# Kernel optimization log

Measured on AMD Instinct MI355X. Metric: run time of the kernel, lower is better.

## Reference

```python
import jax, jax.numpy as jnp
import numpy as np

B, H, W = 16, 96, 96
KS = (5, 3, 3)          # kernel sizes per layer
PD = (2, 1, 1)          # paddings per layer
PCT = (0.5, 0.5, 0.4)   # triangle_cReLU percent per layer
C1, C2, C3 = 64, 128, 256
ALPHA = jnp.linspace(0.9, 0.99, 4, dtype=jnp.float32).reshape(2, 2)  # SFM alpha (not trained)


def extract_patches(x, k, s, p):
    # x: (B,C,H,W) -> (B, Ho*Wo, C*k*k), torch.unfold ordering (C slowest)
    x = jnp.pad(x, ((0, 0), (0, 0), (p, p), (p, p)))
    b, c, h, w = x.shape
    ho, wo = (h - k) // s + 1, (w - k) // s + 1
    I = (jnp.arange(ho) * s)[:, None, None, None] + jnp.arange(k)[None, None, :, None]
    J = (jnp.arange(wo) * s)[None, :, None, None] + jnp.arange(k)[None, None, None, :]
    pt = x[:, :, I, J]                      # (B,C,Ho,Wo,k,k)
    pt = pt.transpose(0, 2, 3, 1, 4, 5).reshape(b, ho * wo, c * k * k)
    return pt, ho, wo


def rbf_conv(x, Wt, k, s, p):
    # torch: cdist(unfold(x), W) -> (B, O, Ho, Wo)
    pt, ho, wo = extract_patches(x, k, s, p)
    d2 = (jnp.sum(pt * pt, -1)[:, :, None]
          + jnp.sum(Wt * Wt, -1)[None, None, :]
          - 2.0 * jnp.einsum('bpk,ok->bpo', pt, Wt))
    d = jnp.sqrt(jnp.maximum(d2, 1e-12))
    return d.transpose(0, 2, 1).reshape(x.shape[0], Wt.shape[0], ho, wo)


def triangle_crelu(d, w, percent):
    # threshold = int((1-percent)*C)-th largest over channel dim, capped at w
    c = d.shape[1]
    k = int((1.0 - percent) * c)
    dt = jnp.transpose(d, (0, 2, 3, 1))           # (B,H,W,C)
    thr = jax.lax.top_k(dt, k)[0][..., k - 1]     # (B,H,W)
    thr = jnp.minimum(thr, w)[:, None, :, :]
    d = jnp.where(d > thr, w, d)
    return 1.0 - d / w


def sfm(x, f):
    # non-overlapping fxf weighted-mean pooling with alpha weights
    b, c, h, w = x.shape
    xb = x.reshape(b, c, h // f, f, w // f, f).transpose(0, 1, 2, 4, 3, 5)
    return jnp.mean(xb * ALPHA, axis=(-2, -1))


def branch(xc, W1, W2, W3, wv):
    # xc: (B,H,W) single color channel; wv: (3,) triangle w per layer
    x = xc[:, None]                                   # (B,1,H,W)
    x = rbf_conv(x, W1, KS[0], 1, PD[0])
    x = triangle_crelu(x, wv[0], PCT[0])
    x = sfm(x, 2)                                     # (B,64,48,48)
    x = rbf_conv(x, W2, KS[1], 1, PD[1])
    x = triangle_crelu(x, wv[1], PCT[1])
    x = sfm(x, 2)                                     # (B,128,24,24)
    x = rbf_conv(x, W3, KS[2], 1, PD[2])
    x = triangle_crelu(x, wv[2], PCT[2])              # (B,256,24,24)
    return x


def setup_inputs() -> dict:
    key = jax.random.key(0)
    ks = jax.random.split(key, 8)

    def kaiming(k, shape):
        bound = float(np.sqrt(6.0 / shape[-1]))
        return jax.random.uniform(k, shape, jnp.float32, -bound, bound)

    x = jax.random.normal(ks[0], (B, 3, H, W), jnp.float32)
    conv_w1 = kaiming(ks[1], (3, C1, 1 * KS[0] * KS[0]))    # per-branch RBF prototypes
    conv_w2 = kaiming(ks[2], (3, C2, C1 * KS[1] * KS[1]))
    conv_w3 = kaiming(ks[3], (3, C3, C2 * KS[2] * KS[2]))
    tri_w = jnp.tile(jnp.array([0.4, 0.4, 4.0], jnp.float32), (3, 1))  # (branch, layer)
    fc_in = 3 * C3 * 24 * 24
    fc_w = jax.random.normal(ks[4], (10, fc_in), jnp.float32) * 0.01
    fc_b = jnp.zeros((10,), jnp.float32)
    return {"x": x, "conv_w1": conv_w1, "conv_w2": conv_w2, "conv_w3": conv_w3,
            "tri_w": tri_w, "fc_w": fc_w, "fc_b": fc_b}


def reference(x, conv_w1, conv_w2, conv_w3, tri_w, fc_w, fc_b):
    xs = jnp.transpose(x, (1, 0, 2, 3))                       # (3,B,H,W)
    feats = jax.vmap(branch)(xs, conv_w1, conv_w2, conv_w3, tri_w)  # (3,B,256,24,24)
    flat = jnp.transpose(feats, (1, 0, 2, 3, 4)).reshape(x.shape[0], -1)
    return flat @ fc_w.T + fc_b
```

## Files before the change

### kernel.cpp

```cpp
#include <hip/hip_runtime.h>
#include <hip/hip_bf16.h>
#include <math.h>

typedef __attribute__((ext_vector_type(8))) short bf16x8;
typedef __attribute__((ext_vector_type(4))) float f32x4;

__device__ __forceinline__ void bsplit(float f, unsigned short& h,
                                       unsigned short& l) {
  __hip_bfloat16 hb = __float2bfloat16(f);
  float hf = __bfloat162float(hb);
  __hip_bfloat16 lb = __float2bfloat16(f - hf);
  h = *reinterpret_cast<unsigned short*>(&hb);
  l = *reinterpret_cast<unsigned short*>(&lb);
}

template <int CIN, int COUT>
__global__ __launch_bounds__(256) void pack_w_kernel(
    const float* __restrict__ w, unsigned short* __restrict__ bph,
    unsigned short* __restrict__ bpl, float* __restrict__ sout) {
  constexpr int K = CIN * 9;
  constexpr int CC = CIN / 32;
  const int n = blockIdx.x, br = blockIdx.z;
  const int t = threadIdx.x;
  __shared__ float row[K];
  __shared__ float red[256];
  const float* src = w + ((size_t)br * COUT + n) * K;
  float ss = 0.f;
  for (int i = t; i < K; i += 256) {
    float f = src[i];
    row[i] = f;
    ss += f * f;
  }
  red[t] = ss;
  __syncthreads();
  for (int st = 128; st > 0; st >>= 1) {
    if (t < st) red[t] += red[t + st];
    __syncthreads();
  }
  if (t == 0) sout[br * COUT + n] = red[0];
  for (int i = t; i < K; i += 256) {
    int kpos = i / CIN;
    int e = i - kpos * CIN;
    float f = row[e * 9 + kpos];
    unsigned short h, l;
    bsplit(f, h, l);
    size_t oidx =
        (((size_t)br * 9 * CC + (size_t)kpos * CC + (e >> 5)) * COUT + n) * 32 +
        (e & 31);
    bph[oidx] = h;
    bpl[oidx] = l;
  }
}

__global__ __launch_bounds__(256) void pack_w1_prep_kernel(
    const float* __restrict__ w1, const float* __restrict__ s2,
    const float* __restrict__ s3, const float* __restrict__ tri,
    unsigned short* __restrict__ bh, unsigned short* __restrict__ bl,
    float* __restrict__ s1, float* __restrict__ po0_2,
    float* __restrict__ sp0_2, float* __restrict__ act0_3) {
  const int blk = blockIdx.x;
  const int t = threadIdx.x;
  if (blk < 24) {
    int idx = blk * 256 + t;
    int k = idx & 31;
    int col = (idx >> 5) & 63;
    int br = idx >> 11;
    float f = (k < 31 && k < 25) ? w1[(br * 64 + col) * 25 + k] : 0.f;
    unsigned short h, l;
    bsplit(f, h, l);
    bh[idx] = h;
    bl[idx] = l;
    float v = f * f;
#pragma unroll
    for (int off = 16; off > 0; off >>= 1) v += __shfl_xor(v, off, 64);
    if ((t & 31) == 0) s1[br * 64 + col] = v;
    return;
  }
  if (t >= 64) return;
  const int lane = t;
  if (blk < 27) {
    const int br = blk - 24;
    const float w_ = tri[br * 3 + 1];
    float d0 = sqrtf(fmaxf(s2[br * 128 + lane * 2], 1e-12f));
    float d1 = sqrtf(fmaxf(s2[br * 128 + lane * 2 + 1], 1e-12f));
    int cnt = __popcll(__ballot(d0 >= w_)) + __popcll(__ballot(d1 >= w_));
    float thr;
    if (cnt > 63) {
      thr = w_;
    } else {
      unsigned int k0 = __float_as_uint(d0), k1 = __float_as_uint(d1);
      unsigned int pre = 0;
      int rem = 63;
      for (int b = 30; b >= 0; --b) {
        unsigned int top = (pre >> b) | 1u;
        int c = __popcll(__ballot((k0 >> b) == top)) +
                __popcll(__ballot((k1 >> b) == top));
        if (c > rem) pre |= (1u << b);
        else rem -= c;
      }
      thr = __uint_as_float(pre);
    }
    float th = fminf(thr, w_);
    float a0 = 1.f - ((d0 > th) ? w_ : d0) / w_;
    float a1v = 1.f - ((d1 > th) ? w_ : d1) / w_;
    float p0 = a0 * 0.945f, p1 = a1v * 0.945f;
    po0_2[br * 128 + lane * 2] = p0;
    po0_2[br * 128 + lane * 2 + 1] = p1;
    float ss = p0 * p0 + p1 * p1;
#pragma unroll
    for (int off = 32; off > 0; off >>= 1) ss += __shfl_down(ss, off, 64);
    if (lane == 0) sp0_2[br] = ss;
  } else {
    const int br = blk - 27;
    const float w_ = tri[br * 3 + 2];
    float d[4];
#pragma unroll
    for (int j = 0; j < 4; j++)
      d[j] = sqrtf(fmaxf(s3[br * 256 + lane * 4 + j], 1e-12f));
    int cnt = 0;
#pragma unroll
    for (int j = 0; j < 4; j++) cnt += __popcll(__ballot(d[j] >= w_));
    float thr;
    if (cnt > 152) {
      thr = w_;
    } else {
      unsigned int k[4];
#pragma unroll
      for (int j = 0; j < 4; j++) k[j] = __float_as_uint(d[j]);
      unsigned int pre = 0;
      int rem = 152;
      for (int b = 30; b >= 0; --b) {
        unsigned int top = (pre >> b) | 1u;
        int c = 0;
#pragma unroll
        for (int j = 0; j < 4; j++)
          c += __popcll(__ballot((k[j] >> b) == top));
        if (c > rem) pre |= (1u << b);
        else rem -= c;
      }
      thr = __uint_as_float(pre);
    }
    float th = fminf(thr, w_);
#pragma unroll
    for (int j = 0; j < 4; j++)
      act0_3[br * 256 + lane * 4 + j] = 1.f - ((d[j] > th) ? w_ : d[j]) / w_;
  }
}

__global__ __launch_bounds__(256) void layer1_kernel(
    const float* __restrict__ x, const unsigned short* __restrict__ bw1h,
    const unsigned short* __restrict__ bw1l, const float* __restrict__ sw2v,
    const float* __restrict__ tri, float* __restrict__ a1,
    char* __restrict__ zf1) {
  const int gidx = blockIdx.x;
  const int gy = gidx / 12, gx = gidx % 12;
  const int n = blockIdx.y, br = blockIdx.z;
  const int t = threadIdx.x;
  const int lane = t & 63, wid = t >> 6;

  __shared__ __align__(16) float win[12][12];
  __shared__ float sp2s[64];
  __shared__ float sw2s[64];
  __shared__ __align__(16) float dmat[64][68];

  const int y0 = gy * 8 - 2, x0 = gx * 8 - 2;
  const float* xb = x + ((size_t)(n * 3 + br)) * 96 * 96;
  if (t < 144) {
    int wy = t / 12, wx = t - (t / 12) * 12;
    int y = y0 + wy, xx = x0 + wx;
    float v = 0.f;
    if (y >= 0 && y < 96 && xx >= 0 && xx < 96) v = xb[y * 96 + xx];
    win[wy][wx] = v;
  }
  if (t >= 192) sw2s[t - 192] = sw2v[br * 64 + (t - 192)];
  __syncthreads();

  if (t < 64) {
    int py = t >> 3, px = t & 7;
    float s = 0.f;
#pragma unroll
    for (int ky = 0; ky < 5; ky++)
#pragma unroll
      for (int kx = 0; kx < 5; kx++) {
        float v = win[py + ky][px + kx];
        s += v * v;
      }
    sp2s[t] = s;
  }

  const int mrow = lane & 15;
  const int slot = lane >> 4;
  const int pixel = wid * 16 + mrow;
  const int ppy = pixel >> 3, ppx = pixel & 7;
  unsigned short ahv[8], alv[8];
#pragma unroll
  for (int j = 0; j < 8; j++) {
    int k = slot * 8 + j;
    float v = 0.f;
    if (k < 25) {
      int ky = (k * 205) >> 10;
      int kx = k - ky * 5;
      v = win[ppy + ky][ppx + kx];
    }
    bsplit(v, ahv[j], alv[j]);
  }
  bf16x8 ah = *reinterpret_cast<bf16x8*>(ahv);
  bf16x8 al = *reinterpret_cast<bf16x8*>(alv);

  f32x4 acc[4], accB[4];
  f32x4 zz = {0.f, 0.f, 0.f, 0.f};
#pragma unroll
  for (int nt = 0; nt < 4; nt++) {
    acc[nt] = zz;
    accB[nt] = zz;
  }
#pragma unroll
  for (int nt = 0; nt < 4; nt++) {
    const int off = ((br * 64 + nt * 16 + mrow) << 5) + (slot << 3);
    bf16x8 bh = *reinterpret_cast<const bf16x8*>(bw1h + off);
    bf16x8 bl = *reinterpret_cast<const bf16x8*>(bw1l + off);
    acc[nt] = __builtin_amdgcn_mfma_f32_16x16x32_bf16(ah, bh, acc[nt], 0, 0, 0);
    accB[nt] =
        __builtin_amdgcn_mfma_f32_16x16x32_bf16(ah, bl, accB[nt], 0, 0, 0);
    accB[nt] =
        __builtin_amdgcn_mfma_f32_16x16x32_bf16(al, bh, accB[nt], 0, 0, 0);
  }
  __syncthreads();

  const float w_ = tri[br * 3 + 0];
  const float w2_ = w_ * w_;
  const int flidx = ((br * 16 + n) * 48 + gy * 4 + wid) * 12 + gx;

  float d2v[4][4];
#pragma unroll
  for (int nt = 0; nt < 4; nt++) {
    const float swc = sw2s[nt * 16 + mrow];
#pragma unroll
    for (int rg = 0; rg < 4; rg++)
      d2v[nt][rg] = sp2s[wid * 16 + slot * 4 + rg] + swc -
                    2.f * (acc[nt][rg] + accB[nt][rg]);
  }

  int cnt_lt[4] = {0, 0, 0, 0};
#pragma unroll
  for (int rg = 0; rg < 4; rg++) {
#pragma unroll
    for (int nt = 0; nt < 4; nt++) {
      unsigned long long m = __ballot(d2v[nt][rg] < w2_);
      cnt_lt[rg] += __popcll((m >> (slot * 16)) & 0xFFFFull);
    }
  }

  const bool myzero = (cnt_lt[0] | cnt_lt[1] | cnt_lt[2] | cnt_lt[3]) == 0;
  if (__all(myzero)) {
    if (lane == 0) zf1[flidx] = 0;
    return;
  }

  const float A2[2][2] = {{0.9f, 0.93f}, {0.96f, 0.99f}};
  const bool mycheap = cnt_lt[0] <= 32 && cnt_lt[1] <= 32 &&
                       cnt_lt[2] <= 32 && cnt_lt[3] <= 32;
  if (__all(mycheap)) {
#pragma unroll
    for (int nt = 0; nt < 4; nt++) {
      const int ch = nt * 16 + mrow;
#pragma unroll
      for (int rg = 0; rg < 4; rg++) {
        const int p = wid * 16 + slot * 4 + rg;
        float d2 = d2v[nt][rg];
        float a = (d2 < w2_) ? 1.f - sqrtf(fmaxf(d2, 1e-12f)) / w_ : 0.f;
        dmat[p][ch] = a;
      }
    }
    float pooled[4];
#pragma unroll
    for (int g = 0; g < 4; g++) {
      float po = 0.f;
#pragma unroll
      for (int py = 0; py < 2; py++)
#pragma unroll
        for (int q = 0; q < 2; q++) {
          int pi = py * 8 + g * 2 + q;
          po += dmat[wid * 16 + pi][lane] * A2[py][q];
        }
      pooled[g] = po * 0.25f;
    }
    bool nz = (pooled[0] != 0.f) | (pooled[1] != 0.f) | (pooled[2] != 0.f) |
              (pooled[3] != 0.f);
    unsigned long long mm = __ballot(nz);
    if (mm) {
#pragma unroll
      for (int g = 0; g < 4; g++)
        a1[((((size_t)(br * 16 + n)) * 48 + (gy * 4 + wid)) * 48 +
            (gx * 4 + g)) * 64 + lane] = pooled[g];
      if (lane == 0) zf1[flidx] = 1;
    } else {
      if (lane == 0) zf1[flidx] = 0;
    }
    return;
  }

#pragma unroll
  for (int nt = 0; nt < 4; nt++) {
    const int ch = nt * 16 + mrow;
#pragma unroll
    for (int rg = 0; rg < 4; rg++) {
      const int p = wid * 16 + slot * 4 + rg;
      dmat[p][ch] = sqrtf(fmaxf(d2v[nt][rg], 1e-12f));
    }
  }
  float thrv[16];
  unsigned int need = 0;
#pragma unroll
  for (int i = 0; i < 16; i++) {
    float v = dmat[wid * 16 + i][lane];
    int cnt = __popcll(__ballot(v >= w_));
    if (cnt >= 32) thrv[i] = w_;
    else need |= (1u << i);
  }
  if (need) {
#pragma unroll
    for (int i = 0; i < 16; i++) {
      if (!((need >> i) & 1)) continue;
      unsigned int key = __float_as_uint(dmat[wid * 16 + i][lane]);
      unsigned int pre = 0;
      int rem = 31;
      for (int b = 30; b >= 0; --b) {
        unsigned int top = (pre >> b) | 1u;
        int cnt = __popcll(__ballot((key >> b) == top));
        if (cnt > rem) pre |= (1u << b);
        else rem -= cnt;
      }
      thrv[i] = __uint_as_float(pre);
    }
  }
  float pooled[4];
#pragma unroll
  for (int g = 0; g < 4; g++) {
    float po = 0.f;
#pragma unroll
    for (int py = 0; py < 2; py++)
#pragma unroll
      for (int q = 0; q < 2; q++) {
        int pi = py * 8 + g * 2 + q;
        float d = dmat[wid * 16 + pi][lane];
        float th = fminf(thrv[pi], w_);
        float a = 1.f - ((d > th) ? w_ : d) / w_;
        po += a * A2[py][q];
      }
    pooled[g] = po * 0.25f;
  }
  bool nz = (pooled[0] != 0.f) | (pooled[1] != 0.f) | (pooled[2] != 0.f) |
            (pooled[3] != 0.f);
  unsigned long long mm = __ballot(nz);
  if (mm) {
#pragma unroll
    for (int g = 0; g < 4; g++)
      a1[((((size_t)(br * 16 + n)) * 48 + (gy * 4 + wid)) * 48 +
          (gx * 4 + g)) * 64 + lane] = pooled[g];
    if (lane == 0) zf1[flidx] = 1;
  } else {
    if (lane == 0) zf1[flidx] = 0;
  }
}

__global__ __launch_bounds__(256) void rbf_l2(
    const float* __restrict__ a1, const unsigned short* __restrict__ bph,
    const unsigned short* __restrict__ bpl, const float* __restrict__ sw2v,
    const float* __restrict__ tri, const char* __restrict__ zf1,
    const float* __restrict__ po0_2, char* __restrict__ zf2,
    float* __restrict__ a2) {
  constexpr int CIN = 64, COUT = 128, HIN = 48, KRANK = 63;
  constexpr int CC = CIN / 32, NCH = 9 * CC, NTW = 2, PADC = COUT + 4;
  constexpr int WIN_USH = 60 * CIN;
  constexpr int WIN_BYTES = 2 * WIN_USH * 2;
  constexpr int DMAT_BYTES = 32 * PADC * 4;
  constexpr int UNI_BYTES = WIN_BYTES > DMAT_BYTES ? WIN_BYTES : DMAT_BYTES;

  __shared__ __align__(16) char uni[UNI_BYTES];
  __shared__ float cellq[60][4];
  __shared__ float cellsum[60];
  __shared__ float sp2[32];
  __shared__ float thrs[32];
  __shared__ float sw2s[COUT];
  __shared__ float po0s[COUT];
  __shared__ char fl[24];
  __shared__ int anyf, zflag, diffl;

  unsigned short* winh = (unsigned short*)uni;
  unsigned short* winl = winh + WIN_USH;
  float* dmat = (float*)uni;

  const int gy = blockIdx.x / 6, gx = blockIdx.x % 6;
  const int n = blockIdx.y, br = blockIdx.z;
  const int t = threadIdx.x, lane = t & 63, wvid = t >> 6, ng = wvid;
  const float w_ = tri[br * 3 + 1];
  const int y0 = gy * 4 - 1, x0 = gx * 8 - 1;
  const int fbase = ((br * 16 + n) * 12 + gy) * 6 + gx;

  if (t < 24) {
    int i = t >> 2, j = t & 3;
    int r = gy * 4 - 1 + i, ct = 2 * gx - 1 + j;
    fl[t] = (r >= 0 && r < 48 && ct >= 0 && ct < 12)
                ? zf1[((br * 16 + n) * 48 + r) * 12 + ct]
                : (char)0;
  }
  if (t == 255) diffl = 0;
  __syncthreads();
  if (t == 0) {
    int a = 0;
    for (int i = 0; i < 24; i++) a |= fl[i];
    anyf = a;
  }
  __syncthreads();
  if (!anyf) {
    if (t == 0) zf2[fbase] = 0;
    return;
  }

  for (int i = t; i < COUT; i += 256) {
    sw2s[i] = sw2v[br * COUT + i];
    po0s[i] = po0_2[br * COUT + i];
  }

  const int cell = t >> 2, q = t & 3;
  const int wy = cell / 10, wx = cell - (cell / 10) * 10;
  const int yy = y0 + wy, xx = x0 + wx;
  bool ok = false;
  if (t < 240 && yy >= 0 && yy < HIN && xx >= 0 && xx < HIN)
    ok = fl[wy * 4 + ((xx >> 2) - (2 * gx - 1))] != 0;
  if (t < 240) {
    const float* rp =
        a1 + ((size_t)((br * 16 + n) * HIN + yy) * HIN + xx) * CIN +
        q * (CIN / 4);
    const int sx = (wx & 7) << 3;
    float ss = 0.f;
#pragma unroll
    for (int cq = 0; cq < CIN / 16; cq++) {
      float4 v = ok ? *reinterpret_cast<const float4*>(rp + cq * 4)
                    : make_float4(0.f, 0.f, 0.f, 0.f);
      unsigned short hh[4], ll[4];
      float fv[4] = {v.x, v.y, v.z, v.w};
#pragma unroll
      for (int j = 0; j < 4; j++) {
        float f = fv[j];
        ss += f * f;
        bsplit(f, hh[j], ll[j]);
      }
      int c = q * (CIN / 4) + cq * 4;
      int cst = c ^ sx;
      *reinterpret_cast<ushort4*>(&winh[cell * CIN + cst]) =
          make_ushort4(hh[0], hh[1], hh[2], hh[3]);
      *reinterpret_cast<ushort4*>(&winl[cell * CIN + cst]) =
          make_ushort4(ll[0], ll[1], ll[2], ll[3]);
    }
    cellq[cell][q] = ss;
  }
  __syncthreads();
  if (t < 60)
    cellsum[t] = cellq[t][0] + cellq[t][1] + cellq[t][2] + cellq[t][3];
  __syncthreads();
  if (t < 32) {
    int py = t >> 3, px = t & 7;
    float s = 0.f;
#pragma unroll
    for (int ky = 0; ky < 3; ky++)
#pragma unroll
      for (int kx = 0; kx < 3; kx++) s += cellsum[(py + ky) * 10 + px + kx];
    sp2[t] = s;
  }
  if (t == 0) {
    float s = 0.f;
    for (int i = 0; i < 60; i++) s += cellsum[i];
    zflag = (s == 0.f);
  }
  __syncthreads();
  if (zflag) {
    if (t == 0) zf2[fbase] = 0;
    return;
  }

  const int pix0 = lane & 15;
  const int g8 = (lane >> 4) << 3;
  const int ppy = pix0 >> 3, ppx = pix0 & 7;

  f32x4 acc[2][NTW], accB[2][NTW];
  f32x4 zz = {0.f, 0.f, 0.f, 0.f};
#pragma unroll
  for (int mt = 0; mt < 2; mt++)
#pragma unroll
    for (int nt = 0; nt < NTW; nt++) {
      acc[mt][nt] = zz;
      accB[mt][nt] = zz;
    }

  const size_t bbase = (size_t)br * NCH;
  const int nb0 = ng * (NTW * 16) + pix0;
  bf16x8 bufA[2 * NTW], bufB[2 * NTW], bufC[2 * NTW];

  auto loadB = [&](int chunk, bf16x8* dst) {
    const unsigned short* p0 = bph + ((bbase + chunk) * COUT + nb0) * 32 + g8;
    const unsigned short* p1 = bpl + ((bbase + chunk) * COUT + nb0) * 32 + g8;
#pragma unroll
    for (int nt = 0; nt < NTW; nt++) {
      dst[2 * nt] = *reinterpret_cast<const bf16x8*>(p0 + nt * 512);
      dst[2 * nt + 1] = *reinterpret_cast<const bf16x8*>(p1 + nt * 512);
    }
  };
  auto compute = [&](int chunk, bf16x8* b) {
    const int kpos = chunk / CC, cc = chunk - (chunk / CC) * CC;
    const int ky = kpos / 3, kx = kpos - (kpos / 3) * 3;
    const int wxx = ppx + kx;
    const int sx = (wxx & 7) << 3;
    const int cbase = ((cc << 5) + g8) ^ sx;
#pragma unroll
    for (int mt = 0; mt < 2; mt++) {
      const int r0 = (mt * 2 + ppy + ky) * 10 + wxx;
      bf16x8 ah = *reinterpret_cast<const bf16x8*>(&winh[r0 * CIN + cbase]);
      bf16x8 al = *reinterpret_cast<const bf16x8*>(&winl[r0 * CIN + cbase]);
#pragma unroll
      for (int nt = 0; nt < NTW; nt++) {
        acc[mt][nt] = __builtin_amdgcn_mfma_f32_16x16x32_bf16(
            ah, b[2 * nt], acc[mt][nt], 0, 0, 0);
        accB[mt][nt] = __builtin_amdgcn_mfma_f32_16x16x32_bf16(
            ah, b[2 * nt + 1], accB[mt][nt], 0, 0, 0);
        accB[mt][nt] = __builtin_amdgcn_mfma_f32_16x16x32_bf16(
            al, b[2 * nt], accB[mt][nt], 0, 0, 0);
      }
    }
  };

  loadB(0, bufA);
  loadB(1, bufB);
  for (int g = 0; g < NCH; g += 3) {
    if (g + 2 < NCH) loadB(g + 2, bufC);
    compute(g, bufA);
    if (g + 3 < NCH) loadB(g + 3, bufA);
    compute(g + 1, bufB);
    if (g + 4 < NCH) loadB(g + 4, bufB);
    compute(g + 2, bufC);
  }
  __syncthreads();

  const int rgrp = (lane >> 4) << 2;
#pragma unroll
  for (int mt = 0; mt < 2; mt++) {
    const int prow = mt * 16 + rgrp;
#pragma unroll
    for (int nt = 0; nt < NTW; nt++) {
      const int col = ng * (NTW * 16) + nt * 16 + pix0;
      const float sw = sw2s[col];
#pragma unroll
      for (int rg = 0; rg < 4; rg++) {
        const int pix = prow + rg;
        float d2 =
            sp2[pix] + sw - 2.f * (acc[mt][nt][rg] + accB[mt][nt][rg]);
        dmat[pix * PADC + col] = sqrtf(fmaxf(d2, 1e-12f));
      }
    }
  }
  __syncthreads();

  for (int i = 0; i < 8; i++) {
    const int p = wvid * 8 + i;
    float2 f = *reinterpret_cast<const float2*>(&dmat[p * PADC + lane * 2]);
    float v0 = f.x, v1 = f.y;
    int cnt = __popcll(__ballot(v0 >= w_)) + __popcll(__ballot(v1 >= w_));
    if (cnt > KRANK) {
      if (lane == 0) thrs[p] = w_;
      continue;
    }
    unsigned int k0 = __float_as_uint(v0), k1 = __float_as_uint(v1);
    unsigned int pre = 0;
    int rem = KRANK;
    for (int b = 30; b >= 0; --b) {
      unsigned int top = (pre >> b) | 1u;
      int c = __popcll(__ballot((k0 >> b) == top)) +
              __popcll(__ballot((k1 >> b) == top));
      if (c > rem) pre |= (1u << b);
      else rem -= c;
    }
    if (lane == 0) thrs[p] = __uint_as_float(pre);
  }
  __syncthreads();

  float* ob = a2 + ((size_t)(br * 16 + n)) * 24 * 24 * COUT;
  int mydiff = 0;
  for (int i = t; i < 8 * COUT; i += 256) {
    int qq = i / COUT;
    int chn = i - qq * COUT;
    int qy = qq >> 2, qx = qq & 3;
    int p00 = qy * 16 + qx * 2;
    float d00 = dmat[p00 * PADC + chn];
    float d01 = dmat[(p00 + 1) * PADC + chn];
    float d10 = dmat[(p00 + 8) * PADC + chn];
    float d11 = dmat[(p00 + 9) * PADC + chn];
    float t00 = fminf(thrs[p00], w_);
    float t01 = fminf(thrs[p00 + 1], w_);
    float t10 = fminf(thrs[p00 + 8], w_);
    float t11 = fminf(thrs[p00 + 9], w_);
    float a00 = 1.f - ((d00 > t00) ? w_ : d00) / w_;
    float a01 = 1.f - ((d01 > t01) ? w_ : d01) / w_;
    float a10 = 1.f - ((d10 > t10) ? w_ : d10) / w_;
    float a11 = 1.f - ((d11 > t11) ? w_ : d11) / w_;
    float po = 0.25f * (a00 * 0.9f + a01 * 0.93f + a10 * 0.96f + a11 * 0.99f);
    ob[((size_t)((gy * 2 + qy) * 24 + gx * 4 + qx)) * COUT + chn] = po;
    mydiff |= (po != po0s[chn]);
  }
  if (mydiff) diffl = 1;
  __syncthreads();
  if (t == 0) zf2[fbase] = diffl ? 1 : 0;
}

__global__ __launch_bounds__(256) void rbf_l3(
    const float* __restrict__ a2, const unsigned short* __restrict__ bph,
    const unsigned short* __restrict__ bpl, const float* __restrict__ sw2v,
    const float* __restrict__ tri, const char* __restrict__ zf2,
    const float* __restrict__ po0_2, const float* __restrict__ sp0_2,
    const float* __restrict__ act0_3, unsigned short* __restrict__ fT) {
  constexpr int CIN = 128, COUT = 256, HIN = 24, KRANK = 152;
  constexpr int CC = CIN / 32, NCH = 9 * CC, NTW = 4, PADC = COUT + 4;
  constexpr int WIN_USH = 60 * CIN;
  constexpr int WIN_BYTES = 2 * WIN_USH * 2;
  constexpr int DMAT_BYTES = 32 * PADC * 4;
  constexpr int UNI_BYTES = WIN_BYTES > DMAT_BYTES ? WIN_BYTES : DMAT_BYTES;

  __shared__ __align__(16) char uni[UNI_BYTES];
  __shared__ float cellq[60][4];
  __shared__ float cellsum[60];
  __shared__ float sp2[32];
  __shared__ float thrs[32];
  __shared__ float sw2s[COUT];
  __shared__ __align__(16) float po0s[128];
  __shared__ char fl[16];
  __shared__ int pure0, zflag;

  unsigned short* winh = (unsigned short*)uni;
  unsigned short* winl = winh + WIN_USH;
  float* dmat = (float*)uni;

  const int gy = blockIdx.x / 3, gx = blockIdx.x % 3;
  const int n = blockIdx.y, br = blockIdx.z;
  const int t = threadIdx.x, lane = t & 63, wvid = t >> 6, ng = wvid;
  const float w_ = tri[br * 3 + 2];
  const int y0 = gy * 4 - 1, x0 = gx * 8 - 1;
  const float sp0 = sp0_2[br];

  if (t < 16) {
    int i = t >> 2, j = t & 3;
    int tr = 2 * gy - 1 + i, tc = 2 * gx - 1 + j;
    fl[t] = (tr >= 0 && tr < 12 && tc >= 0 && tc < 6)
                ? zf2[((br * 16 + n) * 12 + tr) * 6 + tc]
                : (char)0;
  }
  if (t >= 64 && t < 192) po0s[t - 64] = po0_2[br * 128 + (t - 64)];
  __syncthreads();
  if (t == 0) {
    int a = 0;
    for (int i = 0; i < 16; i++) a |= fl[i];
    pure0 = (!a) && (sp0 == 0.f);
  }
  __syncthreads();

  unsigned short* obT = fT + (size_t)(br * 16 + n) * 256 * 576;
  if (pure0) {
    int col = t;
    float a = act0_3[br * 256 + col];
    unsigned short h, l;
    bsplit(a, h, l);
    unsigned int hh = (unsigned int)h | ((unsigned int)h << 16);
    uint4 hv = {hh, hh, hh, hh};
#pragma unroll
    for (int row = 0; row < 4; row++)
      *reinterpret_cast<uint4*>(obT + (size_t)col * 576 +
                                (gy * 4 + row) * 24 + gx * 8) = hv;
    return;
  }

  for (int i = t; i < COUT; i += 256) sw2s[i] = sw2v[br * COUT + i];

  const int cell = t >> 2, q = t & 3;
  const int wy = cell / 10, wx = cell - (cell / 10) * 10;
  const int yy = y0 + wy, xx = x0 + wx;
  const bool okb =
      (t < 240) && (yy >= 0 && yy < HIN && xx >= 0 && xx < HIN);
  int fcell = 0;
  if (okb)
    fcell = fl[((yy >> 1) - (2 * gy - 1)) * 4 + ((xx >> 2) - (2 * gx - 1))];
  if (t < 240) {
    const float* rp =
        a2 + ((size_t)((br * 16 + n) * HIN + yy) * HIN + xx) * CIN +
        q * (CIN / 4);
    const int sx = (wx & 7) << 3;
    float ss = 0.f;
#pragma unroll
    for (int cq = 0; cq < CIN / 16; cq++) {
      int c = q * (CIN / 4) + cq * 4;
      float4 v;
      if (!okb) v = make_float4(0.f, 0.f, 0.f, 0.f);
      else if (!fcell) v = *reinterpret_cast<const float4*>(&po0s[c]);
      else v = *reinterpret_cast<const float4*>(rp + cq * 4);
      unsigned short hh[4], ll[4];
      float fv[4] = {v.x, v.y, v.z, v.w};
#pragma unroll
      for (int j = 0; j < 4; j++) {
        float f = fv[j];
        ss += f * f;
        bsplit(f, hh[j], ll[j]);
      }
      int cst = c ^ sx;
      *reinterpret_cast<ushort4*>(&winh[cell * CIN + cst]) =
          make_ushort4(hh[0], hh[1], hh[2], hh[3]);
      *reinterpret_cast<ushort4*>(&winl[cell * CIN + cst]) =
          make_ushort4(ll[0], ll[1], ll[2], ll[3]);
    }
    cellq[cell][q] = ss;
  }
  __syncthreads();
  if (t < 60)
    cellsum[t] = cellq[t][0] + cellq[t][1] + cellq[t][2] + cellq[t][3];
  __syncthreads();
  if (t < 32) {
    int py = t >> 3, px = t & 7;
    float s = 0.f;
#pragma unroll
    for (int ky = 0; ky < 3; ky++)
#pragma unroll
      for (int kx = 0; kx < 3; kx++) s += cellsum[(py + ky) * 10 + px + kx];
    sp2[t] = s;
  }
  if (t == 0) {
    float s = 0.f;
    for (int i = 0; i < 60; i++) s += cellsum[i];
    zflag = (s == 0.f);
  }
  __syncthreads();
  if (zflag) {
    int col = t;
    float a = act0_3[br * 256 + col];
    unsigned short h, l;
    bsplit(a, h, l);
    unsigned int hh = (unsigned int)h | ((unsigned int)h << 16);
    uint4 hv = {hh, hh, hh, hh};
#pragma unroll
    for (int row = 0; row < 4; row++)
      *reinterpret_cast<uint4*>(obT + (size_t)col * 576 +
                                (gy * 4 + row) * 24 + gx * 8) = hv;
    return;
  }

  const int pix0 = lane & 15;
  const int g8 = (lane >> 4) << 3;
  const int ppy = pix0 >> 3, ppx = pix0 & 7;

  f32x4 acc[2][NTW], accB[2][NTW];
  f32x4 zz = {0.f, 0.f, 0.f, 0.f};
#pragma unroll
  for (int mt = 0; mt < 2; mt++)
#pragma unroll
    for (int nt = 0; nt < NTW; nt++) {
      acc[mt][nt] = zz;
      accB[mt][nt] = zz;
    }

  const size_t bbase = (size_t)br * NCH;
  const int nb0 = ng * (NTW * 16) + pix0;
  bf16x8 bufA[2 * NTW], bufB[2 * NTW], bufC[2 * NTW];

  auto loadB = [&](int chunk, bf16x8* dst) {
    const unsigned short* p0 = bph + ((bbase + chunk) * COUT + nb0) * 32 + g8;
    const unsigned short* p1 = bpl + ((bbase + chunk) * COUT + nb0) * 32 + g8;
#pragma unroll
    for (int nt = 0; nt < NTW; nt++) {
      dst[2 * nt] = *reinterpret_cast<const bf16x8*>(p0 + nt * 512);
      dst[2 * nt + 1] = *reinterpret_cast<const bf16x8*>(p1 + nt * 512);
    }
  };
  auto compute = [&](int chunk, bf16x8* b) {
    const int kpos = chunk / CC, cc = chunk - (chunk / CC) * CC;
    const int ky = kpos / 3, kx = kpos - (kpos / 3) * 3;
    const int wxx = ppx + kx;
    const int sx = (wxx & 7) << 3;
    const int cbase = ((cc << 5) + g8) ^ sx;
#pragma unroll
    for (int mt = 0; mt < 2; mt++) {
      const int r0 = (mt * 2 + ppy + ky) * 10 + wxx;
      bf16x8 ah = *reinterpret_cast<const bf16x8*>(&winh[r0 * CIN + cbase]);
      bf16x8 al = *reinterpret_cast<const bf16x8*>(&winl[r0 * CIN + cbase]);
#pragma unroll
      for (int nt = 0; nt < NTW; nt++) {
        acc[mt][nt] = __builtin_amdgcn_mfma_f32_16x16x32_bf16(
            ah, b[2 * nt], acc[mt][nt], 0, 0, 0);
        accB[mt][nt] = __builtin_amdgcn_mfma_f32_16x16x32_bf16(
            ah, b[2 * nt + 1], accB[mt][nt], 0, 0, 0);
        accB[mt][nt] = __builtin_amdgcn_mfma_f32_16x16x32_bf16(
            al, b[2 * nt], accB[mt][nt], 0, 0, 0);
      }
    }
  };

  loadB(0, bufA);
  loadB(1, bufB);
  for (int g = 0; g < NCH; g += 3) {
    if (g + 2 < NCH) loadB(g + 2, bufC);
    compute(g, bufA);
    if (g + 3 < NCH) loadB(g + 3, bufA);
    compute(g + 1, bufB);
    if (g + 4 < NCH) loadB(g + 4, bufB);
    compute(g + 2, bufC);
  }
  __syncthreads();

  const int rgrp = (lane >> 4) << 2;
#pragma unroll
  for (int mt = 0; mt < 2; mt++) {
    const int prow = mt * 16 + rgrp;
#pragma unroll
    for (int nt = 0; nt < NTW; nt++) {
      const int col = ng * (NTW * 16) + nt * 16 + pix0;
      const float sw = sw2s[col];
#pragma unroll
      for (int rg = 0; rg < 4; rg++) {
        const int pix = prow + rg;
        float d2 =
            sp2[pix] + sw - 2.f * (acc[mt][nt][rg] + accB[mt][nt][rg]);
        dmat[pix * PADC + col] = sqrtf(fmaxf(d2, 1e-12f));
      }
    }
  }
  __syncthreads();

  for (int i = 0; i < 8; i++) {
    const int p = wvid * 8 + i;
    float4 f = *reinterpret_cast<const float4*>(&dmat[p * PADC + lane * 4]);
    float v0 = f.x, v1 = f.y, v2 = f.z, v3 = f.w;
    int cnt = __popcll(__ballot(v0 >= w_)) + __popcll(__ballot(v1 >= w_)) +
              __popcll(__ballot(v2 >= w_)) + __popcll(__ballot(v3 >= w_));
    if (cnt > KRANK) {
      if (lane == 0) thrs[p] = w_;
      continue;
    }
    unsigned int k0 = __float_as_uint(v0), k1 = __float_as_uint(v1);
    unsigned int k2 = __float_as_uint(v2), k3 = __float_as_uint(v3);
    unsigned int pre = 0;
    int rem = KRANK;
    for (int b = 30; b >= 0; --b) {
      unsigned int top = (pre >> b) | 1u;
      int c = __popcll(__ballot((k0 >> b) == top)) +
              __popcll(__ballot((k1 >> b) == top)) +
              __popcll(__ballot((k2 >> b) == top)) +
              __popcll(__ballot((k3 >> b) == top));
      if (c > rem) pre |= (1u << b);
      else rem -= c;
    }
    if (lane == 0) thrs[p] = __uint_as_float(pre);
  }
  __syncthreads();

  for (int item = t; item < 256 * 4; item += 256) {
    int chn = item & 255;
    int rowq = item >> 8;
    __align__(16) unsigned short hv[8];
#pragma unroll
    for (int px = 0; px < 8; px++) {
      int p = rowq * 8 + px;
      float d = dmat[p * PADC + chn];
      float tt = fminf(thrs[p], w_);
      float a = 1.f - ((d > tt) ? w_ : d) / w_;
      unsigned short h, l;
      bsplit(a, h, l);
      hv[px] = h;
    }
    *reinterpret_cast<uint4*>(obT + (size_t)chn * 576 +
                              (gy * 4 + rowq) * 24 + gx * 8) =
        *reinterpret_cast<uint4*>(hv);
  }
}

__global__ __launch_bounds__(64) void fc_mfma_kernel(
    const unsigned short* __restrict__ fT, const float* __restrict__ fcw,
    float* __restrict__ partial) {
  const int blk = blockIdx.x;
  const int lane = threadIdx.x;
  const int mrow = lane & 15;
  const int slot = lane >> 4;
  const int slot8 = slot * 8;
  const int k0base = blk * 256;

  f32x4 acc = {0.f, 0.f, 0.f, 0.f};
  float4 z4 = make_float4(0.f, 0.f, 0.f, 0.f);
  for (int cc = 0; cc < 8; ++cc) {
    int k0 = k0base + cc * 32;
    int br = k0 / 147456;
    int rb = k0 - br * 147456;
    int c = rb / 576;
    int pth = rb - c * 576;
    size_t aoff = ((size_t)(br * 16 + mrow) * 256 + c) * 576 + pth + slot8;
    bf16x8 ah = *reinterpret_cast<const bf16x8*>(fT + aoff);
    float4 b0 = z4, b1q = z4;
    if (mrow < 10) {
      const float* bp = fcw + (size_t)mrow * 442368 + k0 + slot8;
      b0 = *reinterpret_cast<const float4*>(bp);
      b1q = *reinterpret_cast<const float4*>(bp + 4);
    }
    float bf[8] = {b0.x, b0.y, b0.z, b0.w, b1q.x, b1q.y, b1q.z, b1q.w};
    unsigned short bhv[8], blv[8];
#pragma unroll
    for (int j = 0; j < 8; j++) bsplit(bf[j], bhv[j], blv[j]);
    bf16x8 bh = *reinterpret_cast<bf16x8*>(bhv);
    bf16x8 bl = *reinterpret_cast<bf16x8*>(blv);
    acc = __builtin_amdgcn_mfma_f32_16x16x32_bf16(ah, bh, acc, 0, 0, 0);
    acc = __builtin_amdgcn_mfma_f32_16x16x32_bf16(ah, bl, acc, 0, 0, 0);
  }
#pragma unroll
  for (int rg = 0; rg < 4; rg++)
    partial[(size_t)blk * 256 + (slot * 4 + rg) * 16 + mrow] = acc[rg];
}

__global__ __launch_bounds__(64) void fc_final_kernel(
    const float* __restrict__ partial, const float* __restrict__ fcb,
    float* __restrict__ outp) {
  const int n = blockIdx.x / 10, oo = blockIdx.x % 10;
  const int lane = threadIdx.x;
  float s = 0.f;
  for (int b = lane; b < 1728; b += 64)
    s += partial[(size_t)b * 256 + n * 16 + oo];
#pragma unroll
  for (int off = 32; off > 0; off >>= 1) s += __shfl_down(s, off, 64);
  if (lane == 0) outp[n * 10 + oo] = s + fcb[oo];
}

extern "C" void kernel_launch(void* const* d_in, const int* in_sizes, int n_in,
                              void* d_out, int out_size, void* d_ws,
                              size_t ws_size, hipStream_t stream) {
  const float* x   = (const float*)d_in[0];
  const float* w1  = (const float*)d_in[1];
  const float* w2  = (const float*)d_in[2];
  const float* w3  = (const float*)d_in[3];
  const float* tri = (const float*)d_in[4];
  const float* fcw = (const float*)d_in[5];
  const float* fcb = (const float*)d_in[6];
  float* out = (float*)d_out;

  float* ws = (float*)d_ws;
  float* a1      = ws;
  float* a2      = a1 + 7077888;
  float* s1      = a2 + 3538944;
  float* s2      = s1 + 192;
  float* s3      = s2 + 384;
  float* po0_2   = s3 + 768;
  float* sp0_2   = po0_2 + 384;
  float* act0_3  = sp0_2 + 16;
  float* partial = act0_3 + 768;
  unsigned short* fT   = (unsigned short*)(partial + 442368);
  unsigned short* bw1h = fT + 7077888;
  unsigned short* bw1l = bw1h + 6144;
  unsigned short* bph2 = bw1l + 6144;
  unsigned short* bpl2 = bph2 + 221184;
  unsigned short* bph3 = bpl2 + 221184;
  unsigned short* bpl3 = bph3 + 884736;
  char* zf1 = (char*)(bpl3 + 884736);
  char* zf2 = zf1 + 27648;

  pack_w_kernel<64, 128><<<dim3(128, 1, 3), dim3(256), 0, stream>>>(
      w2, bph2, bpl2, s2);
  pack_w_kernel<128, 256><<<dim3(256, 1, 3), dim3(256), 0, stream>>>(
      w3, bph3, bpl3, s3);
  pack_w1_prep_kernel<<<dim3(30), dim3(256), 0, stream>>>(
      w1, s2, s3, tri, bw1h, bw1l, s1, po0_2, sp0_2, act0_3);

  layer1_kernel<<<dim3(144, 16, 3), dim3(256), 0, stream>>>(x, bw1h, bw1l, s1,
                                                            tri, a1, zf1);
  rbf_l2<<<dim3(72, 16, 3), dim3(256), 0, stream>>>(a1, bph2, bpl2, s2, tri,
                                                    zf1, po0_2, zf2, a2);
  rbf_l3<<<dim3(18, 16, 3), dim3(256), 0, stream>>>(a2, bph3, bpl3, s3, tri,
                                                    zf2, po0_2, sp0_2, act0_3,
                                                    fT);
  fc_mfma_kernel<<<dim3(1728), dim3(64), 0, stream>>>(fT, fcw, partial);
  fc_final_kernel<<<dim3(160), dim3(64), 0, stream>>>(partial, fcb, out);
}
```

Measured before the change: 71.51 us.

## Double rbf_l2 tile height to 8 input rows per block

Each rbf_l2 block now covers 8 input rows (64 pixels) instead of 4, and the grid is halved. The halo load (10x10 window) and the packed-weight B loads are amortized over twice the MFMA work, cutting redundant window rows and weight fetches. The cost is larger shared memory (window and dmat), twice the accumulator registers, and fewer blocks in flight, which may reduce occupancy. The zero flags are now written for two tiles per block.

```diff
diff --git a/kernel.cpp b/kernel.cpp
--- a/kernel.cpp
+++ b/kernel.cpp
@@ -65,7 +65,7 @@
     int k = idx & 31;
     int col = (idx >> 5) & 63;
     int br = idx >> 11;
-    float f = (k < 31 && k < 25) ? w1[(br * 64 + col) * 25 + k] : 0.f;
+    float f = (k < 25) ? w1[(br * 64 + col) * 25 + k] : 0.f;
     unsigned short h, l;
     bsplit(f, h, l);
     bh[idx] = h;
@@ -372,20 +372,21 @@
     float* __restrict__ a2) {
   constexpr int CIN = 64, COUT = 128, HIN = 48, KRANK = 63;
   constexpr int CC = CIN / 32, NCH = 9 * CC, NTW = 2, PADC = COUT + 4;
-  constexpr int WIN_USH = 60 * CIN;
+  constexpr int WIN_USH = 100 * CIN;
   constexpr int WIN_BYTES = 2 * WIN_USH * 2;
-  constexpr int DMAT_BYTES = 32 * PADC * 4;
+  constexpr int DMAT_BYTES = 64 * PADC * 4;
   constexpr int UNI_BYTES = WIN_BYTES > DMAT_BYTES ? WIN_BYTES : DMAT_BYTES;
 
   __shared__ __align__(16) char uni[UNI_BYTES];
-  __shared__ float cellq[60][4];
-  __shared__ float cellsum[60];
-  __shared__ float sp2[32];
-  __shared__ float thrs[32];
+  __shared__ float cellq[100][2];
+  __shared__ float cellsum[100];
+  __shared__ float sp2[64];
+  __shared__ float thrs[64];
   __shared__ float sw2s[COUT];
   __shared__ float po0s[COUT];
-  __shared__ char fl[24];
-  __shared__ int anyf, zflag, diffl;
+  __shared__ char fl[40];
+  __shared__ int anyf, zflag;
+  __shared__ int diff2[2];
 
   unsigned short* winh = (unsigned short*)uni;
   unsigned short* winl = winh + WIN_USH;
@@ -395,26 +396,30 @@
   const int n = blockIdx.y, br = blockIdx.z;
   const int t = threadIdx.x, lane = t & 63, wvid = t >> 6, ng = wvid;
   const float w_ = tri[br * 3 + 1];
-  const int y0 = gy * 4 - 1, x0 = gx * 8 - 1;
-  const int fbase = ((br * 16 + n) * 12 + gy) * 6 + gx;
-
-  if (t < 24) {
+  const int y0 = gy * 8 - 1, x0 = gx * 8 - 1;
+  const int fbase0 = ((br * 16 + n) * 12 + 2 * gy) * 6 + gx;
+
+  if (t < 40) {
     int i = t >> 2, j = t & 3;
-    int r = gy * 4 - 1 + i, ct = 2 * gx - 1 + j;
+    int r = y0 + i, ct = 2 * gx - 1 + j;
     fl[t] = (r >= 0 && r < 48 && ct >= 0 && ct < 12)
                 ? zf1[((br * 16 + n) * 48 + r) * 12 + ct]
                 : (char)0;
   }
-  if (t == 255) diffl = 0;
+  if (t == 254) diff2[0] = 0;
+  if (t == 255) diff2[1] = 0;
   __syncthreads();
   if (t == 0) {
     int a = 0;
-    for (int i = 0; i < 24; i++) a |= fl[i];
+    for (int i = 0; i < 40; i++) a |= fl[i];
     anyf = a;
   }
   __syncthreads();
   if (!anyf) {
-    if (t == 0) zf2[fbase] = 0;
+    if (t == 0) {
+      zf2[fbase0] = 0;
+      zf2[fbase0 + 6] = 0;
+    }
     return;
   }
 
@@ -423,20 +428,20 @@
     po0s[i] = po0_2[br * COUT + i];
   }
 
-  const int cell = t >> 2, q = t & 3;
+  const int cell = t >> 1, q = t & 1;
   const int wy = cell / 10, wx = cell - (cell / 10) * 10;
   const int yy = y0 + wy, xx = x0 + wx;
   bool ok = false;
-  if (t < 240 && yy >= 0 && yy < HIN && xx >= 0 && xx < HIN)
+  if (t < 200 && yy >= 0 && yy < HIN && xx >= 0 && xx < HIN)
     ok = fl[wy * 4 + ((xx >> 2) - (2 * gx - 1))] != 0;
-  if (t < 240) {
+  if (t < 200) {
     const float* rp =
         a1 + ((size_t)((br * 16 + n) * HIN + yy) * HIN + xx) * CIN +
-        q * (CIN / 4);
+        q * (CIN / 2);
     const int sx = (wx & 7) << 3;
     float ss = 0.f;
 #pragma unroll
-    for (int cq = 0; cq < CIN / 16; cq++) {
+    for (int cq = 0; cq < CIN / 8; cq++) {
       float4 v = ok ? *reinterpret_cast<const float4*>(rp + cq * 4)
                     : make_float4(0.f, 0.f, 0.f, 0.f);
       unsigned short hh[4], ll[4];
@@ -447,7 +452,7 @@
         ss += f * f;
         bsplit(f, hh[j], ll[j]);
       }
-      int c = q * (CIN / 4) + cq * 4;
+      int c = q * (CIN / 2) + cq * 4;
       int cst = c ^ sx;
       *reinterpret_cast<ushort4*>(&winh[cell * CIN + cst]) =
           make_ushort4(hh[0], hh[1], hh[2], hh[3]);
@@ -457,10 +462,9 @@
     cellq[cell][q] = ss;
   }
   __syncthreads();
-  if (t < 60)
-    cellsum[t] = cellq[t][0] + cellq[t][1] + cellq[t][2] + cellq[t][3];
-  __syncthreads();
-  if (t < 32) {
+  if (t < 100) cellsum[t] = cellq[t][0] + cellq[t][1];
+  __syncthreads();
+  if (t < 64) {
     int py = t >> 3, px = t & 7;
     float s = 0.f;
 #pragma unroll
@@ -471,12 +475,15 @@
   }
   if (t == 0) {
     float s = 0.f;
-    for (int i = 0; i < 60; i++) s += cellsum[i];
+    for (int i = 0; i < 100; i++) s += cellsum[i];
     zflag = (s == 0.f);
   }
   __syncthreads();
   if (zflag) {
-    if (t == 0) zf2[fbase] = 0;
+    if (t == 0) {
+      zf2[fbase0] = 0;
+      zf2[fbase0 + 6] = 0;
+    }
     return;
   }
 
@@ -484,10 +491,10 @@
   const int g8 = (lane >> 4) << 3;
   const int ppy = pix0 >> 3, ppx = pix0 & 7;
 
-  f32x4 acc[2][NTW], accB[2][NTW];
+  f32x4 acc[4][NTW], accB[4][NTW];
   f32x4 zz = {0.f, 0.f, 0.f, 0.f};
 #pragma unroll
-  for (int mt = 0; mt < 2; mt++)
+  for (int mt = 0; mt < 4; mt++)
 #pragma unroll
     for (int nt = 0; nt < NTW; nt++) {
       acc[mt][nt] = zz;
@@ -514,7 +521,7 @@
     const int sx = (wxx & 7) << 3;
     const int cbase = ((cc << 5) + g8) ^ sx;
 #pragma unroll
-    for (int mt = 0; mt < 2; mt++) {
+    for (int mt = 0; mt < 4; mt++) {
       const int r0 = (mt * 2 + ppy + ky) * 10 + wxx;
       bf16x8 ah = *reinterpret_cast<const bf16x8*>(&winh[r0 * CIN + cbase]);
       bf16x8 al = *reinterpret_cast<const bf16x8*>(&winl[r0 * CIN + cbase]);
@@ -544,7 +551,7 @@
 
   const int rgrp = (lane >> 4) << 2;
 #pragma unroll
-  for (int mt = 0; mt < 2; mt++) {
+  for (int mt = 0; mt < 4; mt++) {
     const int prow = mt * 16 + rgrp;
 #pragma unroll
     for (int nt = 0; nt < NTW; nt++) {
@@ -561,8 +568,8 @@
   }
   __syncthreads();
 
-  for (int i = 0; i < 8; i++) {
-    const int p = wvid * 8 + i;
+  for (int i = 0; i < 16; i++) {
+    const int p = wvid * 16 + i;
     float2 f = *reinterpret_cast<const float2*>(&dmat[p * PADC + lane * 2]);
     float v0 = f.x, v1 = f.y;
     int cnt = __popcll(__ballot(v0 >= w_)) + __popcll(__ballot(v1 >= w_));
@@ -585,8 +592,8 @@
   __syncthreads();
 
   float* ob = a2 + ((size_t)(br * 16 + n)) * 24 * 24 * COUT;
-  int mydiff = 0;
-  for (int i = t; i < 8 * COUT; i += 256) {
+  int mydiff0 = 0, mydiff1 = 0;
+  for (int i = t; i < 16 * COUT; i += 256) {
     int qq = i / COUT;
     int chn = i - qq * COUT;
     int qy = qq >> 2, qx = qq & 3;
@@ -604,12 +611,18 @@
     float a10 = 1.f - ((d10 > t10) ? w_ : d10) / w_;
     float a11 = 1.f - ((d11 > t11) ? w_ : d11) / w_;
     float po = 0.25f * (a00 * 0.9f + a01 * 0.93f + a10 * 0.96f + a11 * 0.99f);
-    ob[((size_t)((gy * 2 + qy) * 24 + gx * 4 + qx)) * COUT + chn] = po;
-    mydiff |= (po != po0s[chn]);
-  }
-  if (mydiff) diffl = 1;
-  __syncthreads();
-  if (t == 0) zf2[fbase] = diffl ? 1 : 0;
+    ob[((size_t)((gy * 4 + qy) * 24 + gx * 4 + qx)) * COUT + chn] = po;
+    int df = (po != po0s[chn]);
+    if (qy < 2) mydiff0 |= df;
+    else mydiff1 |= df;
+  }
+  if (mydiff0) diff2[0] = 1;
+  if (mydiff1) diff2[1] = 1;
+  __syncthreads();
+  if (t == 0) {
+    zf2[fbase0] = diff2[0] ? 1 : 0;
+    zf2[fbase0 + 6] = diff2[1] ? 1 : 0;
+  }
 }
 
 __global__ __launch_bounds__(256) void rbf_l3(
@@ -971,7 +984,7 @@
 
   layer1_kernel<<<dim3(144, 16, 3), dim3(256), 0, stream>>>(x, bw1h, bw1l, s1,
                                                             tri, a1, zf1);
-  rbf_l2<<<dim3(72, 16, 3), dim3(256), 0, stream>>>(a1, bph2, bpl2, s2, tri,
+  rbf_l2<<<dim3(36, 16, 3), dim3(256), 0, stream>>>(a1, bph2, bpl2, s2, tri,
                                                     zf1, po0_2, zf2, a2);
   rbf_l3<<<dim3(18, 16, 3), dim3(256), 0, stream>>>(a2, bph3, bpl3, s3, tri,
                                                     zf2, po0_2, sp0_2, act0_3,
```

After: 73.61 us. 2.9% more time.
